# Performance work log

Measured on AMD Instinct MI355X. Metric: run time of the kernel, lower is better.

The kernel has to match this reference:

```python
import jax, jax.numpy as jnp
import numpy as np

B, N, F_IN, OUT_FEATS, NUM_CLS, NUM_INDS = 256, 200, 200, 256, 8, 512
PCT_EDGES = 20
K = int(PCT_EDGES / 100 * N * (N - 1) / 2)  # 3980 hard edges
TAU = 1.0


def setup_inputs() -> dict:
    key = jax.random.key(0)
    ks = jax.random.split(key, 6)
    x = jax.random.normal(ks[0], (B, N, F_IN), dtype=jnp.float32)
    gumbel_u = jax.random.uniform(ks[1], (B, N, N), dtype=jnp.float32)
    nets = jax.random.normal(ks[2], (NUM_INDS, N, N), dtype=jnp.float32)
    w_gnn = jax.random.normal(ks[3], (F_IN, OUT_FEATS), dtype=jnp.float32) / np.sqrt(F_IN).astype(np.float32)
    w_lin = jax.random.normal(ks[4], (OUT_FEATS, NUM_CLS), dtype=jnp.float32) / np.sqrt(OUT_FEATS).astype(np.float32)
    b_lin = jnp.zeros((NUM_CLS,), dtype=jnp.float32)
    net_index = jax.random.randint(ks[5], (B,), 0, NUM_INDS)
    return {"x": x, "gumbel_u": gumbel_u, "nets": nets, "w_gnn": w_gnn,
            "w_lin": w_lin, "b_lin": b_lin, "net_index": net_index}


def _gumbel_softkmax(logits, u, k, tau):
    # logits: [B, N, N]; u: uniform(0,1) noise -> Gumbel(0,1) via -log(-log(u))
    b, n, _ = logits.shape
    g = -jnp.log(-jnp.log(jnp.clip(u, 1e-10, 1.0 - 1e-10)))
    g = (logits + g) / tau
    sym = (g + jnp.swapaxes(g, 1, 2)) * 0.5                      # symmetrize
    y_soft = jax.nn.softmax(sym.reshape(b, -1), axis=-1).reshape(b, n, n)
    upper_flat = jnp.triu(y_soft).reshape(b, -1)                 # upper tri incl. diag
    _, idx = jax.lax.top_k(upper_flat, k)                        # [B, k]
    y_hard = jnp.zeros_like(upper_flat).at[jnp.arange(b)[:, None], idx].set(1.0)
    y_hard = y_hard.reshape(b, n, n)
    diag = jnp.diagonal(y_hard, axis1=-2, axis2=-1)              # [B, N]
    eye = jnp.eye(n, dtype=y_hard.dtype)
    y_hard = y_hard + jnp.swapaxes(y_hard, 1, 2) - diag[:, :, None] * eye
    # straight-through estimator
    return y_hard - jax.lax.stop_gradient(y_soft) + y_soft


def reference(x, gumbel_u, nets, w_gnn, w_lin, b_lin, net_index):
    selected = nets[net_index]                                   # [B, N, N]
    adj = _gumbel_softkmax(selected, gumbel_u, K, TAU)
    # gnn: relu(adj @ x @ W_gnn)  -> embeddings [B, N, OUT_FEATS]
    emb = jax.nn.relu(jnp.einsum('bij,bjf,fo->bio', adj, x, w_gnn))
    out = emb @ w_lin + b_lin                                    # [B, N, NUM_CLS]
    return out, emb, adj
```

## Files before the change

### kernel.cpp

```cpp
#include <hip/hip_runtime.h>
#include <math.h>

#define B_SZ 256
#define N_SZ 200
#define NN (N_SZ * N_SZ)
#define FIN 200
#define OUT_F 256
#define NCLS 8
#define KSEL 3980
#define NUPPER 20100
#define KSTRIDE 20128
#define NT 7
#define NTILES 28
#define CAND_CAP 2048

#define ADJ_STRIDE 224
#define KGRP_PB 25
#define XWM_PB (KGRP_PB * 2048)

#define EMB_OFF (B_SZ * N_SZ * NCLS)
#define ADJ_OFF (EMB_OFF + B_SZ * N_SZ * OUT_F)

#define KEYS_OFF_B   0
#define SEL_OFF_B    21659648
#define CCNT_OFF_B   21661696
#define CAND_OFF_B   21662720
#define WKG_OFF_B    26214400
#define ADJB16_OFF_B 26329088

typedef unsigned short ushort_t;
typedef float f32x4 __attribute__((ext_vector_type(4)));
typedef short bf16x8 __attribute__((ext_vector_type(8)));

__device__ __forceinline__ unsigned sortkey(float f) {
    unsigned u = __float_as_uint(f);
    return (u & 0x80000000u) ? ~u : (u | 0x80000000u);
}

__device__ __forceinline__ ushort_t f2b(float f) {
    unsigned u = __float_as_uint(f);
    return (ushort_t)((u + 0x7FFFu + ((u >> 16) & 1u)) >> 16);
}

__device__ __forceinline__ bf16x8 f2b8(float4 lo, float4 hi) {
    bf16x8 r;
    r[0] = (short)f2b(lo.x); r[1] = (short)f2b(lo.y);
    r[2] = (short)f2b(lo.z); r[3] = (short)f2b(lo.w);
    r[4] = (short)f2b(hi.x); r[5] = (short)f2b(hi.y);
    r[6] = (short)f2b(hi.z); r[7] = (short)f2b(hi.w);
    return r;
}

__device__ __forceinline__ void tile_decode(int t, int& ti, int& tj) {
    int a = 0, rem = t;
    while (rem >= NT - a) { rem -= NT - a; ++a; }
    ti = a; tj = a + rem;
}

__global__ __launch_bounds__(256) void kA(
    const float* __restrict__ gu, const float* __restrict__ nets,
    const int* __restrict__ net_index, unsigned* __restrict__ keys)
{
    const int blk = blockIdx.x;
    const int b = blk / NTILES;
    int ti, tj; tile_decode(blk % NTILES, ti, tj);
    const int i0 = ti * 32, j0 = tj * 32;
    const float* ub = gu + (size_t)b * NN;
    const float* lb = nets + (size_t)net_index[b] * NN;

    __shared__ float Hij[32][33];
    __shared__ float Hji[32][33];

    const int r = threadIdx.x >> 5;
    const int c = threadIdx.x & 31;

    #pragma unroll
    for (int s = 0; s < 4; ++s) {
        int rr = r + 8 * s;
        int i = i0 + rr, j = j0 + c;
        if (i < N_SZ && j < N_SZ) {
            float u = ub[i * N_SZ + j];
            u = fminf(fmaxf(u, 1e-10f), 1.0f - 1e-10f);
            Hij[rr][c] = lb[i * N_SZ + j] - logf(-logf(u));
        }
        if (ti != tj) {
            int i2 = j0 + rr, j2 = i0 + c;
            if (i2 < N_SZ && j2 < N_SZ) {
                float u = ub[i2 * N_SZ + j2];
                u = fminf(fmaxf(u, 1e-10f), 1.0f - 1e-10f);
                Hji[rr][c] = lb[i2 * N_SZ + j2] - logf(-logf(u));
            }
        }
    }
    __syncthreads();

    unsigned* kb = keys + (size_t)b * KSTRIDE;
    #pragma unroll
    for (int s = 0; s < 4; ++s) {
        int rr = r + 8 * s;
        int i = i0 + rr, j = j0 + c;
        if (i < N_SZ && j < N_SZ && i <= j) {
            float hji = (ti == tj) ? Hij[c][rr] : Hji[c][rr];
            float sv = 0.5f * (Hij[rr][c] + hji);
            int base = i * N_SZ - (i * (i - 1)) / 2;
            kb[base + (j - i)] = sortkey(sv);
        }
    }
}

__global__ __launch_bounds__(256) void kFinal(
    const unsigned* __restrict__ keys, unsigned* __restrict__ sel)
{
    const int b = blockIdx.x;
    const int tid = threadIdx.x;
    __shared__ unsigned kl[NUPPER];
    __shared__ unsigned hist[256];
    __shared__ unsigned sfx[256];
    __shared__ unsigned sPrefix;
    __shared__ int sKK;

    const unsigned* kb = keys + (size_t)b * KSTRIDE;
    for (int idx = tid; idx < NUPPER; idx += 256) kl[idx] = kb[idx];

    unsigned prefix = 0;
    int kk = KSEL;
    for (int round = 0; round < 4; ++round) {
        const int shift = 24 - 8 * round;
        hist[tid] = 0;
        __syncthreads();
        for (int idx = tid; idx < NUPPER; idx += 256) {
            unsigned key = kl[idx];
            bool in = (round == 0) || ((key >> (shift + 8)) == prefix);
            if (in) atomicAdd(&hist[(key >> shift) & 255u], 1u);
        }
        __syncthreads();
        sfx[tid] = hist[tid];
        __syncthreads();
        #pragma unroll
        for (int off = 1; off < 256; off <<= 1) {
            unsigned add = (tid + off < 256) ? sfx[tid + off] : 0u;
            __syncthreads();
            sfx[tid] += add;
            __syncthreads();
        }
        unsigned above = (tid < 255) ? sfx[tid + 1] : 0u;
        if (sfx[tid] >= (unsigned)kk && above < (unsigned)kk) {
            sPrefix = (prefix << 8) | (unsigned)tid;
            sKK = kk - (int)above;
        }
        __syncthreads();
        prefix = sPrefix;
        kk = sKK;
        __syncthreads();
    }
    if (tid == 0) {
        sel[b * 2] = prefix;
        sel[b * 2 + 1] = (unsigned)kk;
    }
}

__global__ __launch_bounds__(256) void kW(
    const unsigned* __restrict__ keys, const unsigned* __restrict__ sel,
    unsigned* __restrict__ candCnt, unsigned* __restrict__ cand,
    float* __restrict__ out_base, ushort_t* __restrict__ adjb16)
{
    const int blk = blockIdx.x;
    const int b = blk / NTILES;
    int ti, tj; tile_decode(blk % NTILES, ti, tj);
    const int i0 = ti * 32, j0 = tj * 32;
    const unsigned kth = sel[b * 2];
    const unsigned* kb = keys + (size_t)b * KSTRIDE;
    float* adj = out_base + ADJ_OFF + (size_t)b * NN;
    ushort_t* ab = adjb16 + (size_t)b * (N_SZ * ADJ_STRIDE);

    __shared__ float V[32][33];
    const int r = threadIdx.x >> 5;
    const int c = threadIdx.x & 31;

    #pragma unroll
    for (int s = 0; s < 4; ++s) {
        int rr = r + 8 * s;
        int i = i0 + rr, j = j0 + c;
        if (i < N_SZ && j < N_SZ && i <= j) {
            int base = i * N_SZ - (i * (i - 1)) / 2;
            unsigned key = kb[base + (j - i)];
            float v = (key > kth) ? 1.0f : 0.0f;
            if (key == kth) {
                unsigned p = atomicAdd(&candCnt[b], 1u);
                if (p < CAND_CAP) cand[(size_t)b * CAND_CAP + p] = (unsigned)(i * N_SZ + j);
            }
            V[rr][c] = v;
            if (ti == tj) V[c][rr] = v;
        }
    }
    __syncthreads();
    #pragma unroll
    for (int s = 0; s < 4; ++s) {
        int rr = r + 8 * s;
        int i = i0 + rr, j = j0 + c;
        if (i < N_SZ) {
            float v = (j < N_SZ) ? V[rr][c] : 0.0f;
            if (j < N_SZ) adj[i * N_SZ + j] = v;
            ab[i * ADJ_STRIDE + j] = (v != 0.0f) ? (ushort_t)0x3F80 : (ushort_t)0;
        }
    }
    if (ti != tj) {
        #pragma unroll
        for (int s = 0; s < 4; ++s) {
            int rr = r + 8 * s;
            int i2 = j0 + rr, j2 = i0 + c;
            if (i2 < N_SZ) {
                float v = V[c][rr];
                adj[i2 * N_SZ + j2] = v;
                ab[i2 * ADJ_STRIDE + j2] = (v != 0.0f) ? (ushort_t)0x3F80 : (ushort_t)0;
            }
        }
    }
}

__global__ void kT(const unsigned* __restrict__ sel,
                   const unsigned* __restrict__ candCnt,
                   const unsigned* __restrict__ cand,
                   float* __restrict__ out_base, ushort_t* __restrict__ adjb16)
{
    const int b = blockIdx.x;
    if (threadIdx.x != 0) return;
    int kk = (int)sel[b * 2 + 1];
    int cnt = (int)candCnt[b];
    if (cnt > CAND_CAP) cnt = CAND_CAP;
    float* adj = out_base + ADJ_OFF + (size_t)b * NN;
    ushort_t* ab = adjb16 + (size_t)b * (N_SZ * ADJ_STRIDE);
    int take = kk < cnt ? kk : cnt;
    unsigned used[64];
    int nu = 0;
    for (int t = 0; t < take; ++t) {
        unsigned best = 0xFFFFFFFFu;
        for (int q = 0; q < cnt; ++q) {
            unsigned v = cand[(size_t)b * CAND_CAP + q];
            bool skip = false;
            for (int u = 0; u < nu; ++u) if (used[u] == v) { skip = true; break; }
            if (!skip && v < best) best = v;
        }
        if (best == 0xFFFFFFFFu) break;
        if (nu < 64) used[nu++] = best;
        int i = (int)(best / N_SZ), j = (int)(best % N_SZ);
        adj[i * N_SZ + j] = 1.0f;
        adj[j * N_SZ + i] = 1.0f;
        ab[i * ADJ_STRIDE + j] = (ushort_t)0x3F80;
        ab[j * ADJ_STRIDE + i] = (ushort_t)0x3F80;
    }
}

__global__ __launch_bounds__(256) void kWprep(
    const float* __restrict__ wg, ushort_t* __restrict__ wkg,
    unsigned* __restrict__ candCnt)
{
    if (blockIdx.x == 0) candCnt[threadIdx.x] = 0;
    int e = blockIdx.x * 256 + threadIdx.x;
    int kg = e >> 11;
    int rem = e & 2047;
    int n = rem >> 3;
    int ki = rem & 7;
    int k = kg * 8 + ki;
    wkg[e] = (k < FIN) ? f2b(wg[k * OUT_F + n]) : (ushort_t)0;
}

__global__ __launch_bounds__(256) void k2_mfma(
    const float* __restrict__ x, const ushort_t* __restrict__ wkg,
    ushort_t* __restrict__ xwm)
{
    const int r0 = blockIdx.x * 64;
    const int tid = threadIdx.x;
    const int w = tid >> 6;
    const int l = tid & 63;
    const int g = l >> 4;
    const int r = l & 15;

    __shared__ __align__(16) ushort_t Cs[64 * 256];

    f32x4 acc[4][4];
    #pragma unroll
    for (int mf = 0; mf < 4; ++mf)
        #pragma unroll
        for (int nf = 0; nf < 4; ++nf)
            acc[mf][nf] = (f32x4){0.f, 0.f, 0.f, 0.f};

    for (int c = 0; c < 7; ++c) {
        const int koff = (c * 32 + g * 8 < FIN) ? (c * 32 + g * 8) : 0;
        bf16x8 af[4], bf[4];
        #pragma unroll
        for (int mf = 0; mf < 4; ++mf) {
            const float* ap = x + (size_t)(r0 + mf * 16 + r) * FIN + koff;
            float4 lo = *(const float4*)ap;
            float4 hi = *(const float4*)(ap + 4);
            af[mf] = f2b8(lo, hi);
        }
        #pragma unroll
        for (int nf = 0; nf < 4; ++nf)
            bf[nf] = *(const bf16x8*)(wkg + c * 8192 + g * 2048 + (w * 64 + nf * 16 + r) * 8);
        #pragma unroll
        for (int mf = 0; mf < 4; ++mf)
            #pragma unroll
            for (int nf = 0; nf < 4; ++nf)
                acc[mf][nf] = __builtin_amdgcn_mfma_f32_16x16x32_bf16(
                    af[mf], bf[nf], acc[mf][nf], 0, 0, 0);
    }

    #pragma unroll
    for (int mf = 0; mf < 4; ++mf) {
        #pragma unroll
        for (int jj = 0; jj < 4; ++jj) {
            int row = mf * 16 + g * 4 + jj;
            #pragma unroll
            for (int nf = 0; nf < 4; ++nf) {
                int col = w * 64 + nf * 16 + r;
                Cs[((row >> 3) << 11) + col * 8 + (row & 7)] = f2b(acc[mf][nf][jj]);
            }
        }
    }
    __syncthreads();
    #pragma unroll
    for (int kg = 0; kg < 8; ++kg) {
        int grow0 = r0 + kg * 8;
        int bb = grow0 / N_SZ;
        int jb = grow0 % N_SZ;
        ushort_t* dst = xwm + (size_t)bb * XWM_PB + ((jb >> 3) << 11);
        *(int4*)(dst + tid * 8) = *(const int4*)(Cs + (kg << 11) + tid * 8);
    }
}

__global__ __launch_bounds__(256) void k3_fused(
    const ushort_t* __restrict__ adjb16, const ushort_t* __restrict__ xwm,
    const float* __restrict__ wl, const float* __restrict__ bl,
    float* __restrict__ out_base)
{
    const int blk = blockIdx.x;
    const int xcd = blk & 7;
    const int idx = blk >> 3;
    const int b = xcd + 8 * (idx / 7);
    const int mt = idx % 7;
    const int tid = threadIdx.x;
    const int w = tid >> 6;
    const int l = tid & 63;
    const int g = l >> 4;
    const int r = l & 15;

    const ushort_t* adjb = adjb16 + (size_t)b * (N_SZ * ADJ_STRIDE);
    const ushort_t* xwb = xwm + (size_t)b * XWM_PB;

    __shared__ float red[4][4][8][8];

    int arow0 = mt * 32 + r;       if (arow0 > N_SZ - 1) arow0 = N_SZ - 1;
    int arow1 = mt * 32 + 16 + r;  if (arow1 > N_SZ - 1) arow1 = N_SZ - 1;
    bf16x8 aa[2][7];
    #pragma unroll
    for (int c = 0; c < 7; ++c) {
        aa[0][c] = *(const bf16x8*)(adjb + arow0 * ADJ_STRIDE + c * 32 + g * 8);
        aa[1][c] = *(const bf16x8*)(adjb + arow1 * ADJ_STRIDE + c * 32 + g * 8);
    }

    f32x4 acc[2][4];
    #pragma unroll
    for (int mf = 0; mf < 2; ++mf)
        #pragma unroll
        for (int nf = 0; nf < 4; ++nf)
            acc[mf][nf] = (f32x4){0.f, 0.f, 0.f, 0.f};

    #pragma unroll
    for (int c = 0; c < 7; ++c) {
        bf16x8 bf[4];
        #pragma unroll
        for (int nf = 0; nf < 4; ++nf)
            bf[nf] = *(const bf16x8*)(xwb + c * 8192 + g * 2048 + (w * 64 + nf * 16 + r) * 8);
        #pragma unroll
        for (int mf = 0; mf < 2; ++mf)
            #pragma unroll
            for (int nf = 0; nf < 4; ++nf)
                acc[mf][nf] = __builtin_amdgcn_mfma_f32_16x16x32_bf16(
                    aa[mf][c], bf[nf], acc[mf][nf], 0, 0, 0);
    }

    float wlv[4][NCLS];
    #pragma unroll
    for (int nf = 0; nf < 4; ++nf) {
        int col = w * 64 + nf * 16 + r;
        #pragma unroll
        for (int cls = 0; cls < NCLS; ++cls) wlv[nf][cls] = wl[col * NCLS + cls];
    }

    #pragma unroll
    for (int mf = 0; mf < 2; ++mf) {
        #pragma unroll
        for (int j = 0; j < 4; ++j) {
            int rowl = mf * 16 + g * 4 + j;
            int grow = mt * 32 + rowl;
            float e0 = fmaxf(acc[mf][0][j], 0.0f);
            float e1 = fmaxf(acc[mf][1][j], 0.0f);
            float e2 = fmaxf(acc[mf][2][j], 0.0f);
            float e3 = fmaxf(acc[mf][3][j], 0.0f);
            if (grow < N_SZ) {
                size_t rbase = EMB_OFF + ((size_t)b * N_SZ + grow) * OUT_F;
                out_base[rbase + w * 64 + r]      = e0;
                out_base[rbase + w * 64 + 16 + r] = e1;
                out_base[rbase + w * 64 + 32 + r] = e2;
                out_base[rbase + w * 64 + 48 + r] = e3;
            }
            float pr[NCLS];
            #pragma unroll
            for (int cls = 0; cls < NCLS; ++cls)
                pr[cls] = e0 * wlv[0][cls] + e1 * wlv[1][cls]
                        + e2 * wlv[2][cls] + e3 * wlv[3][cls];
            #pragma unroll
            for (int off = 1; off <= 8; off <<= 1) {
                #pragma unroll
                for (int cls = 0; cls < NCLS; ++cls)
                    pr[cls] += __shfl_xor(pr[cls], off, 64);
            }
            if (r < NCLS) red[w][g][mf * 4 + j][r] = pr[r];
        }
    }
    __syncthreads();

    {
        int rowl = tid >> 3, cls = tid & 7;
        int mf = rowl >> 4, rem = rowl & 15, gg = rem >> 2, jj = rem & 3;
        int slot = mf * 4 + jj;
        int grow = mt * 32 + rowl;
        if (grow < N_SZ) {
            float s = red[0][gg][slot][cls] + red[1][gg][slot][cls]
                    + red[2][gg][slot][cls] + red[3][gg][slot][cls] + bl[cls];
            out_base[((size_t)b * N_SZ + grow) * NCLS + cls] = s;
        }
    }
}

extern "C" void kernel_launch(void* const* d_in, const int* in_sizes, int n_in,
                              void* d_out, int out_size, void* d_ws, size_t ws_size,
                              hipStream_t stream) {
    const float* x    = (const float*)d_in[0];
    const float* gu   = (const float*)d_in[1];
    const float* nets = (const float*)d_in[2];
    const float* wg   = (const float*)d_in[3];
    const float* wl   = (const float*)d_in[4];
    const float* bl   = (const float*)d_in[5];
    const int*   nidx = (const int*)d_in[6];
    float* out = (float*)d_out;

    char* ws = (char*)d_ws;
    unsigned* keys    = (unsigned*)(ws + KEYS_OFF_B);
    unsigned* sel     = (unsigned*)(ws + SEL_OFF_B);
    unsigned* candCnt = (unsigned*)(ws + CCNT_OFF_B);
    unsigned* cand    = (unsigned*)(ws + CAND_OFF_B);
    ushort_t* xwm     = (ushort_t*)(ws + KEYS_OFF_B);
    ushort_t* wkg     = (ushort_t*)(ws + WKG_OFF_B);
    ushort_t* adjb16  = (ushort_t*)(ws + ADJB16_OFF_B);

    kWprep<<<224, 256, 0, stream>>>(wg, wkg, candCnt);
    kA<<<B_SZ * NTILES, 256, 0, stream>>>(gu, nets, nidx, keys);
    kFinal<<<B_SZ, 256, 0, stream>>>(keys, sel);
    kW<<<B_SZ * NTILES, 256, 0, stream>>>(keys, sel, candCnt, cand, out, adjb16);
    kT<<<B_SZ, 64, 0, stream>>>(sel, candCnt, cand, out, adjb16);

    k2_mfma<<<(B_SZ * N_SZ) / 64, 256, 0, stream>>>(x, wkg, xwm);
    k3_fused<<<B_SZ * 7, 256, 0, stream>>>(adjb16, xwm, wl, bl, out);
}
```

Before: 153.3 us.

## Fuse weight prep into kA, vectorize adjacency writes, stage embedding stores via LDS

```diff
diff --git a/kernel.cpp b/kernel.cpp
--- a/kernel.cpp
+++ b/kernel.cpp
@@ -31,6 +31,7 @@
 typedef unsigned short ushort_t;
 typedef float f32x4 __attribute__((ext_vector_type(4)));
 typedef short bf16x8 __attribute__((ext_vector_type(8)));
+typedef ushort_t u16x4 __attribute__((ext_vector_type(4)));
 
 __device__ __forceinline__ unsigned sortkey(float f) {
     unsigned u = __float_as_uint(f);
@@ -59,9 +60,23 @@
 
 __global__ __launch_bounds__(256) void kA(
     const float* __restrict__ gu, const float* __restrict__ nets,
-    const int* __restrict__ net_index, unsigned* __restrict__ keys)
+    const int* __restrict__ net_index, unsigned* __restrict__ keys,
+    const float* __restrict__ wg, ushort_t* __restrict__ wkg,
+    unsigned* __restrict__ candCnt)
 {
     const int blk = blockIdx.x;
+    if (blk >= B_SZ * NTILES) {
+        int pb = blk - B_SZ * NTILES;
+        if (pb == 0) candCnt[threadIdx.x] = 0;
+        int e = pb * 256 + threadIdx.x;
+        int kg = e >> 11;
+        int rem = e & 2047;
+        int n = rem >> 3;
+        int ki = rem & 7;
+        int k = kg * 8 + ki;
+        wkg[e] = (k < FIN) ? f2b(wg[k * OUT_F + n]) : (ushort_t)0;
+        return;
+    }
     const int b = blk / NTILES;
     int ti, tj; tile_decode(blk % NTILES, ti, tj);
     const int i0 = ti * 32, j0 = tj * 32;
@@ -194,26 +209,49 @@
         }
     }
     __syncthreads();
-    #pragma unroll
-    for (int s = 0; s < 4; ++s) {
-        int rr = r + 8 * s;
-        int i = i0 + rr, j = j0 + c;
+
+    const int tr = threadIdx.x >> 3;
+    const int tc = threadIdx.x & 7;
+    {
+        int i = i0 + tr;
         if (i < N_SZ) {
-            float v = (j < N_SZ) ? V[rr][c] : 0.0f;
-            if (j < N_SZ) adj[i * N_SZ + j] = v;
-            ab[i * ADJ_STRIDE + j] = (v != 0.0f) ? (ushort_t)0x3F80 : (ushort_t)0;
+            int jb = j0 + tc * 4;
+            float v0 = (jb + 0 < N_SZ) ? V[tr][tc * 4 + 0] : 0.0f;
+            float v1 = (jb + 1 < N_SZ) ? V[tr][tc * 4 + 1] : 0.0f;
+            float v2 = (jb + 2 < N_SZ) ? V[tr][tc * 4 + 2] : 0.0f;
+            float v3 = (jb + 3 < N_SZ) ? V[tr][tc * 4 + 3] : 0.0f;
+            if (jb + 3 < N_SZ) {
+                float4 v4 = {v0, v1, v2, v3};
+                *(float4*)(adj + (size_t)i * N_SZ + jb) = v4;
+            } else {
+                if (jb + 0 < N_SZ) adj[(size_t)i * N_SZ + jb + 0] = v0;
+                if (jb + 1 < N_SZ) adj[(size_t)i * N_SZ + jb + 1] = v1;
+                if (jb + 2 < N_SZ) adj[(size_t)i * N_SZ + jb + 2] = v2;
+            }
+            u16x4 a4;
+            a4[0] = (v0 != 0.0f) ? (ushort_t)0x3F80 : (ushort_t)0;
+            a4[1] = (v1 != 0.0f) ? (ushort_t)0x3F80 : (ushort_t)0;
+            a4[2] = (v2 != 0.0f) ? (ushort_t)0x3F80 : (ushort_t)0;
+            a4[3] = (v3 != 0.0f) ? (ushort_t)0x3F80 : (ushort_t)0;
+            *(u16x4*)(ab + (size_t)i * ADJ_STRIDE + jb) = a4;
         }
     }
     if (ti != tj) {
-        #pragma unroll
-        for (int s = 0; s < 4; ++s) {
-            int rr = r + 8 * s;
-            int i2 = j0 + rr, j2 = i0 + c;
-            if (i2 < N_SZ) {
-                float v = V[c][rr];
-                adj[i2 * N_SZ + j2] = v;
-                ab[i2 * ADJ_STRIDE + j2] = (v != 0.0f) ? (ushort_t)0x3F80 : (ushort_t)0;
-            }
+        int i2 = j0 + tr;
+        if (i2 < N_SZ) {
+            int jb = i0 + tc * 4;
+            float v0 = V[tc * 4 + 0][tr];
+            float v1 = V[tc * 4 + 1][tr];
+            float v2 = V[tc * 4 + 2][tr];
+            float v3 = V[tc * 4 + 3][tr];
+            float4 v4 = {v0, v1, v2, v3};
+            *(float4*)(adj + (size_t)i2 * N_SZ + jb) = v4;
+            u16x4 a4;
+            a4[0] = (v0 != 0.0f) ? (ushort_t)0x3F80 : (ushort_t)0;
+            a4[1] = (v1 != 0.0f) ? (ushort_t)0x3F80 : (ushort_t)0;
+            a4[2] = (v2 != 0.0f) ? (ushort_t)0x3F80 : (ushort_t)0;
+            a4[3] = (v3 != 0.0f) ? (ushort_t)0x3F80 : (ushort_t)0;
+            *(u16x4*)(ab + (size_t)i2 * ADJ_STRIDE + jb) = a4;
         }
     }
 }
@@ -251,20 +289,6 @@
     }
 }
 
-__global__ __launch_bounds__(256) void kWprep(
-    const float* __restrict__ wg, ushort_t* __restrict__ wkg,
-    unsigned* __restrict__ candCnt)
-{
-    if (blockIdx.x == 0) candCnt[threadIdx.x] = 0;
-    int e = blockIdx.x * 256 + threadIdx.x;
-    int kg = e >> 11;
-    int rem = e & 2047;
-    int n = rem >> 3;
-    int ki = rem & 7;
-    int k = kg * 8 + ki;
-    wkg[e] = (k < FIN) ? f2b(wg[k * OUT_F + n]) : (ushort_t)0;
-}
-
 __global__ __launch_bounds__(256) void k2_mfma(
     const float* __restrict__ x, const ushort_t* __restrict__ wkg,
     ushort_t* __restrict__ xwm)
@@ -348,7 +372,8 @@
     const ushort_t* adjb = adjb16 + (size_t)b * (N_SZ * ADJ_STRIDE);
     const ushort_t* xwb = xwm + (size_t)b * XWM_PB;
 
-    __shared__ float red[4][4][8][8];
+    __shared__ __align__(16) float Es[32 * 256];
+    float (*red)[4][8][8] = (float(*)[4][8][8])Es;
 
     int arow0 = mt * 32 + r;       if (arow0 > N_SZ - 1) arow0 = N_SZ - 1;
     int arow1 = mt * 32 + 16 + r;  if (arow1 > N_SZ - 1) arow1 = N_SZ - 1;
@@ -380,6 +405,30 @@
                     aa[mf][c], bf[nf], acc[mf][nf], 0, 0, 0);
     }
 
+    #pragma unroll
+    for (int mf = 0; mf < 2; ++mf) {
+        #pragma unroll
+        for (int j = 0; j < 4; ++j) {
+            int rowl = mf * 16 + g * 4 + j;
+            #pragma unroll
+            for (int nf = 0; nf < 4; ++nf)
+                Es[rowl * 256 + w * 64 + nf * 16 + r] = fmaxf(acc[mf][nf][j], 0.0f);
+        }
+    }
+    __syncthreads();
+    #pragma unroll
+    for (int q = 0; q < 8; ++q) {
+        int e = q * 256 + tid;
+        int rowl = e >> 6;
+        int c4 = e & 63;
+        int grow = mt * 32 + rowl;
+        if (grow < N_SZ) {
+            float4 v = *(const float4*)(Es + rowl * 256 + c4 * 4);
+            *(float4*)(out_base + EMB_OFF + ((size_t)b * N_SZ + grow) * OUT_F + c4 * 4) = v;
+        }
+    }
+    __syncthreads();
+
     float wlv[4][NCLS];
     #pragma unroll
     for (int nf = 0; nf < 4; ++nf) {
@@ -387,24 +436,14 @@
         #pragma unroll
         for (int cls = 0; cls < NCLS; ++cls) wlv[nf][cls] = wl[col * NCLS + cls];
     }
-
     #pragma unroll
     for (int mf = 0; mf < 2; ++mf) {
         #pragma unroll
         for (int j = 0; j < 4; ++j) {
-            int rowl = mf * 16 + g * 4 + j;
-            int grow = mt * 32 + rowl;
             float e0 = fmaxf(acc[mf][0][j], 0.0f);
             float e1 = fmaxf(acc[mf][1][j], 0.0f);
             float e2 = fmaxf(acc[mf][2][j], 0.0f);
             float e3 = fmaxf(acc[mf][3][j], 0.0f);
-            if (grow < N_SZ) {
-                size_t rbase = EMB_OFF + ((size_t)b * N_SZ + grow) * OUT_F;
-                out_base[rbase + w * 64 + r]      = e0;
-                out_base[rbase + w * 64 + 16 + r] = e1;
-                out_base[rbase + w * 64 + 32 + r] = e2;
-                out_base[rbase + w * 64 + 48 + r] = e3;
-            }
             float pr[NCLS];
             #pragma unroll
             for (int cls = 0; cls < NCLS; ++cls)
@@ -455,8 +494,7 @@
     ushort_t* wkg     = (ushort_t*)(ws + WKG_OFF_B);
     ushort_t* adjb16  = (ushort_t*)(ws + ADJB16_OFF_B);
 
-    kWprep<<<224, 256, 0, stream>>>(wg, wkg, candCnt);
-    kA<<<B_SZ * NTILES, 256, 0, stream>>>(gu, nets, nidx, keys);
+    kA<<<B_SZ * NTILES + 224, 256, 0, stream>>>(gu, nets, nidx, keys, wg, wkg, candCnt);
     kFinal<<<B_SZ, 256, 0, stream>>>(keys, sel);
     kW<<<B_SZ * NTILES, 256, 0, stream>>>(keys, sel, candCnt, cand, out, adjb16);
     kT<<<B_SZ, 64, 0, stream>>>(sel, candCnt, cand, out, adjb16);
```

Result: faster. 148.4 us (-3.2%).

## Fuse top-k selection with adjacency write and shrink GNN tiles

Applied to the files above, without the earlier changes.

```diff
diff --git a/kernel.cpp b/kernel.cpp
--- a/kernel.cpp
+++ b/kernel.cpp
@@ -12,7 +12,6 @@
 #define KSTRIDE 20128
 #define NT 7
 #define NTILES 28
-#define CAND_CAP 2048
 
 #define ADJ_STRIDE 224
 #define KGRP_PB 25
@@ -22,15 +21,14 @@
 #define ADJ_OFF (EMB_OFF + B_SZ * N_SZ * OUT_F)
 
 #define KEYS_OFF_B   0
-#define SEL_OFF_B    21659648
-#define CCNT_OFF_B   21661696
-#define CAND_OFF_B   21662720
 #define WKG_OFF_B    26214400
 #define ADJB16_OFF_B 26329088
 
 typedef unsigned short ushort_t;
 typedef float f32x4 __attribute__((ext_vector_type(4)));
 typedef short bf16x8 __attribute__((ext_vector_type(8)));
+typedef ushort_t u16x4 __attribute__((ext_vector_type(4)));
+typedef ushort_t u16x8 __attribute__((ext_vector_type(8)));
 
 __device__ __forceinline__ unsigned sortkey(float f) {
     unsigned u = __float_as_uint(f);
@@ -59,9 +57,21 @@
 
 __global__ __launch_bounds__(256) void kA(
     const float* __restrict__ gu, const float* __restrict__ nets,
-    const int* __restrict__ net_index, unsigned* __restrict__ keys)
+    const int* __restrict__ net_index, unsigned* __restrict__ keys,
+    const float* __restrict__ wg, ushort_t* __restrict__ wkg)
 {
     const int blk = blockIdx.x;
+    if (blk >= B_SZ * NTILES) {
+        int pb = blk - B_SZ * NTILES;
+        int e = pb * 256 + threadIdx.x;
+        int kg = e >> 11;
+        int rem = e & 2047;
+        int n = rem >> 3;
+        int ki = rem & 7;
+        int k = kg * 8 + ki;
+        wkg[e] = (k < FIN) ? f2b(wg[k * OUT_F + n]) : (ushort_t)0;
+        return;
+    }
     const int b = blk / NTILES;
     int ti, tj; tile_decode(blk % NTILES, ti, tj);
     const int i0 = ti * 32, j0 = tj * 32;
@@ -108,161 +118,121 @@
     }
 }
 
-__global__ __launch_bounds__(256) void kFinal(
-    const unsigned* __restrict__ keys, unsigned* __restrict__ sel)
+__global__ __launch_bounds__(512) void kSelW(
+    const unsigned* __restrict__ keys, float* __restrict__ out_base,
+    ushort_t* __restrict__ adjb16)
 {
     const int b = blockIdx.x;
     const int tid = threadIdx.x;
-    __shared__ unsigned kl[NUPPER];
+    __shared__ __align__(16) unsigned kl[NUPPER];
     __shared__ unsigned hist[256];
     __shared__ unsigned sfx[256];
+    __shared__ unsigned scanA[512];
     __shared__ unsigned sPrefix;
     __shared__ int sKK;
 
-    const unsigned* kb = keys + (size_t)b * KSTRIDE;
-    for (int idx = tid; idx < NUPPER; idx += 256) kl[idx] = kb[idx];
+    {
+        const int4* kb4 = (const int4*)(keys + (size_t)b * KSTRIDE);
+        int4* kl4 = (int4*)kl;
+        for (int q = tid; q < 5025; q += 512) kl4[q] = kb4[q];
+    }
 
     unsigned prefix = 0;
     int kk = KSEL;
     for (int round = 0; round < 4; ++round) {
         const int shift = 24 - 8 * round;
-        hist[tid] = 0;
-        __syncthreads();
-        for (int idx = tid; idx < NUPPER; idx += 256) {
+        if (tid < 256) hist[tid] = 0;
+        __syncthreads();
+        for (int idx = tid; idx < NUPPER; idx += 512) {
             unsigned key = kl[idx];
             bool in = (round == 0) || ((key >> (shift + 8)) == prefix);
             if (in) atomicAdd(&hist[(key >> shift) & 255u], 1u);
         }
         __syncthreads();
-        sfx[tid] = hist[tid];
+        if (tid < 256) sfx[tid] = hist[tid];
         __syncthreads();
         #pragma unroll
         for (int off = 1; off < 256; off <<= 1) {
-            unsigned add = (tid + off < 256) ? sfx[tid + off] : 0u;
+            unsigned add = 0;
+            if (tid < 256 && tid + off < 256) add = sfx[tid + off];
             __syncthreads();
-            sfx[tid] += add;
+            if (tid < 256) sfx[tid] += add;
             __syncthreads();
         }
-        unsigned above = (tid < 255) ? sfx[tid + 1] : 0u;
-        if (sfx[tid] >= (unsigned)kk && above < (unsigned)kk) {
-            sPrefix = (prefix << 8) | (unsigned)tid;
-            sKK = kk - (int)above;
+        if (tid < 256) {
+            unsigned above = (tid < 255) ? sfx[tid + 1] : 0u;
+            if (sfx[tid] >= (unsigned)kk && above < (unsigned)kk) {
+                sPrefix = (prefix << 8) | (unsigned)tid;
+                sKK = kk - (int)above;
+            }
         }
         __syncthreads();
         prefix = sPrefix;
         kk = sKK;
         __syncthreads();
     }
-    if (tid == 0) {
-        sel[b * 2] = prefix;
-        sel[b * 2 + 1] = (unsigned)kk;
-    }
-}
-
-__global__ __launch_bounds__(256) void kW(
-    const unsigned* __restrict__ keys, const unsigned* __restrict__ sel,
-    unsigned* __restrict__ candCnt, unsigned* __restrict__ cand,
-    float* __restrict__ out_base, ushort_t* __restrict__ adjb16)
-{
-    const int blk = blockIdx.x;
-    const int b = blk / NTILES;
-    int ti, tj; tile_decode(blk % NTILES, ti, tj);
-    const int i0 = ti * 32, j0 = tj * 32;
-    const unsigned kth = sel[b * 2];
-    const unsigned* kb = keys + (size_t)b * KSTRIDE;
+    const unsigned kth = prefix;
+
+    const int lo = tid * 40;
+    const int hi = (lo + 40 < NUPPER) ? lo + 40 : NUPPER;
+    unsigned mycnt = 0;
+    for (int idx = lo; idx < hi; ++idx)
+        if (kl[idx] == kth) ++mycnt;
+    scanA[tid] = mycnt;
+    __syncthreads();
+    #pragma unroll
+    for (int off = 1; off < 512; off <<= 1) {
+        unsigned add = (tid >= off) ? scanA[tid - off] : 0u;
+        __syncthreads();
+        scanA[tid] += add;
+        __syncthreads();
+    }
+    unsigned rank = scanA[tid] - mycnt;
+    for (int idx = lo; idx < hi; ++idx) {
+        unsigned key = kl[idx];
+        unsigned dec;
+        if (key > kth) dec = 1u;
+        else if (key == kth) { dec = (rank < (unsigned)kk) ? 1u : 0u; ++rank; }
+        else dec = 0u;
+        kl[idx] = dec;
+    }
+    __syncthreads();
+
     float* adj = out_base + ADJ_OFF + (size_t)b * NN;
+    for (int e = tid; e < 10000; e += 512) {
+        int i = e / 50;
+        int j0 = (e % 50) * 4;
+        int bi = i * N_SZ - (i * (i - 1)) / 2 - i;
+        float4 v;
+        float* vp = (float*)&v;
+        #pragma unroll
+        for (int q = 0; q < 4; ++q) {
+            int j = j0 + q;
+            int pk = (i <= j) ? (bi + j)
+                              : (j * N_SZ - (j * (j - 1)) / 2 + (i - j));
+            vp[q] = kl[pk] ? 1.0f : 0.0f;
+        }
+        *(float4*)(adj + (size_t)i * N_SZ + j0) = v;
+    }
     ushort_t* ab = adjb16 + (size_t)b * (N_SZ * ADJ_STRIDE);
-
-    __shared__ float V[32][33];
-    const int r = threadIdx.x >> 5;
-    const int c = threadIdx.x & 31;
-
-    #pragma unroll
-    for (int s = 0; s < 4; ++s) {
-        int rr = r + 8 * s;
-        int i = i0 + rr, j = j0 + c;
-        if (i < N_SZ && j < N_SZ && i <= j) {
-            int base = i * N_SZ - (i * (i - 1)) / 2;
-            unsigned key = kb[base + (j - i)];
-            float v = (key > kth) ? 1.0f : 0.0f;
-            if (key == kth) {
-                unsigned p = atomicAdd(&candCnt[b], 1u);
-                if (p < CAND_CAP) cand[(size_t)b * CAND_CAP + p] = (unsigned)(i * N_SZ + j);
+    for (int e = tid; e < 5600; e += 512) {
+        int i = e / 28;
+        int j0 = (e % 28) * 8;
+        int bi = i * N_SZ - (i * (i - 1)) / 2 - i;
+        u16x8 v;
+        #pragma unroll
+        for (int q = 0; q < 8; ++q) {
+            int j = j0 + q;
+            ushort_t o = 0;
+            if (j < N_SZ) {
+                int pk = (i <= j) ? (bi + j)
+                                  : (j * N_SZ - (j * (j - 1)) / 2 + (i - j));
+                o = kl[pk] ? (ushort_t)0x3F80 : (ushort_t)0;
             }
-            V[rr][c] = v;
-            if (ti == tj) V[c][rr] = v;
-        }
-    }
-    __syncthreads();
-    #pragma unroll
-    for (int s = 0; s < 4; ++s) {
-        int rr = r + 8 * s;
-        int i = i0 + rr, j = j0 + c;
-        if (i < N_SZ) {
-            float v = (j < N_SZ) ? V[rr][c] : 0.0f;
-            if (j < N_SZ) adj[i * N_SZ + j] = v;
-            ab[i * ADJ_STRIDE + j] = (v != 0.0f) ? (ushort_t)0x3F80 : (ushort_t)0;
-        }
-    }
-    if (ti != tj) {
-        #pragma unroll
-        for (int s = 0; s < 4; ++s) {
-            int rr = r + 8 * s;
-            int i2 = j0 + rr, j2 = i0 + c;
-            if (i2 < N_SZ) {
-                float v = V[c][rr];
-                adj[i2 * N_SZ + j2] = v;
-                ab[i2 * ADJ_STRIDE + j2] = (v != 0.0f) ? (ushort_t)0x3F80 : (ushort_t)0;
-            }
-        }
-    }
-}
-
-__global__ void kT(const unsigned* __restrict__ sel,
-                   const unsigned* __restrict__ candCnt,
-                   const unsigned* __restrict__ cand,
-                   float* __restrict__ out_base, ushort_t* __restrict__ adjb16)
-{
-    const int b = blockIdx.x;
-    if (threadIdx.x != 0) return;
-    int kk = (int)sel[b * 2 + 1];
-    int cnt = (int)candCnt[b];
-    if (cnt > CAND_CAP) cnt = CAND_CAP;
-    float* adj = out_base + ADJ_OFF + (size_t)b * NN;
-    ushort_t* ab = adjb16 + (size_t)b * (N_SZ * ADJ_STRIDE);
-    int take = kk < cnt ? kk : cnt;
-    unsigned used[64];
-    int nu = 0;
-    for (int t = 0; t < take; ++t) {
-        unsigned best = 0xFFFFFFFFu;
-        for (int q = 0; q < cnt; ++q) {
-            unsigned v = cand[(size_t)b * CAND_CAP + q];
-            bool skip = false;
-            for (int u = 0; u < nu; ++u) if (used[u] == v) { skip = true; break; }
-            if (!skip && v < best) best = v;
-        }
-        if (best == 0xFFFFFFFFu) break;
-        if (nu < 64) used[nu++] = best;
-        int i = (int)(best / N_SZ), j = (int)(best % N_SZ);
-        adj[i * N_SZ + j] = 1.0f;
-        adj[j * N_SZ + i] = 1.0f;
-        ab[i * ADJ_STRIDE + j] = (ushort_t)0x3F80;
-        ab[j * ADJ_STRIDE + i] = (ushort_t)0x3F80;
-    }
-}
-
-__global__ __launch_bounds__(256) void kWprep(
-    const float* __restrict__ wg, ushort_t* __restrict__ wkg,
-    unsigned* __restrict__ candCnt)
-{
-    if (blockIdx.x == 0) candCnt[threadIdx.x] = 0;
-    int e = blockIdx.x * 256 + threadIdx.x;
-    int kg = e >> 11;
-    int rem = e & 2047;
-    int n = rem >> 3;
-    int ki = rem & 7;
-    int k = kg * 8 + ki;
-    wkg[e] = (k < FIN) ? f2b(wg[k * OUT_F + n]) : (ushort_t)0;
+            v[q] = o;
+        }
+        *(u16x8*)(ab + (size_t)i * ADJ_STRIDE + j0) = v;
+    }
 }
 
 __global__ __launch_bounds__(256) void k2_mfma(
@@ -337,8 +307,8 @@
     const int blk = blockIdx.x;
     const int xcd = blk & 7;
     const int idx = blk >> 3;
-    const int b = xcd + 8 * (idx / 7);
-    const int mt = idx % 7;
+    const int b = xcd + 8 * (idx / 13);
+    const int mt = idx % 13;
     const int tid = threadIdx.x;
     const int w = tid >> 6;
     const int l = tid & 63;
@@ -348,23 +318,18 @@
     const ushort_t* adjb = adjb16 + (size_t)b * (N_SZ * ADJ_STRIDE);
     const ushort_t* xwb = xwm + (size_t)b * XWM_PB;
 
-    __shared__ float red[4][4][8][8];
-
-    int arow0 = mt * 32 + r;       if (arow0 > N_SZ - 1) arow0 = N_SZ - 1;
-    int arow1 = mt * 32 + 16 + r;  if (arow1 > N_SZ - 1) arow1 = N_SZ - 1;
-    bf16x8 aa[2][7];
-    #pragma unroll
-    for (int c = 0; c < 7; ++c) {
-        aa[0][c] = *(const bf16x8*)(adjb + arow0 * ADJ_STRIDE + c * 32 + g * 8);
-        aa[1][c] = *(const bf16x8*)(adjb + arow1 * ADJ_STRIDE + c * 32 + g * 8);
-    }
-
-    f32x4 acc[2][4];
-    #pragma unroll
-    for (int mf = 0; mf < 2; ++mf)
-        #pragma unroll
-        for (int nf = 0; nf < 4; ++nf)
-            acc[mf][nf] = (f32x4){0.f, 0.f, 0.f, 0.f};
+    __shared__ __align__(16) float Es[16 * 256];
+    float (*red)[4][4][8] = (float(*)[4][4][8])Es;
+
+    int arow = mt * 16 + r; if (arow > N_SZ - 1) arow = N_SZ - 1;
+    bf16x8 aa[7];
+    #pragma unroll
+    for (int c = 0; c < 7; ++c)
+        aa[c] = *(const bf16x8*)(adjb + arow * ADJ_STRIDE + c * 32 + g * 8);
+
+    f32x4 acc[4];
+    #pragma unroll
+    for (int nf = 0; nf < 4; ++nf) acc[nf] = (f32x4){0.f, 0.f, 0.f, 0.f};
 
     #pragma unroll
     for (int c = 0; c < 7; ++c) {
@@ -373,12 +338,31 @@
         for (int nf = 0; nf < 4; ++nf)
             bf[nf] = *(const bf16x8*)(xwb + c * 8192 + g * 2048 + (w * 64 + nf * 16 + r) * 8);
         #pragma unroll
-        for (int mf = 0; mf < 2; ++mf)
-            #pragma unroll
-            for (int nf = 0; nf < 4; ++nf)
-                acc[mf][nf] = __builtin_amdgcn_mfma_f32_16x16x32_bf16(
-                    aa[mf][c], bf[nf], acc[mf][nf], 0, 0, 0);
-    }
+        for (int nf = 0; nf < 4; ++nf)
+            acc[nf] = __builtin_amdgcn_mfma_f32_16x16x32_bf16(
+                aa[c], bf[nf], acc[nf], 0, 0, 0);
+    }
+
+    #pragma unroll
+    for (int j = 0; j < 4; ++j) {
+        int rowl = g * 4 + j;
+        #pragma unroll
+        for (int nf = 0; nf < 4; ++nf)
+            Es[rowl * 256 + w * 64 + nf * 16 + r] = fmaxf(acc[nf][j], 0.0f);
+    }
+    __syncthreads();
+    #pragma unroll
+    for (int q = 0; q < 4; ++q) {
+        int e = q * 256 + tid;
+        int rowl = e >> 6;
+        int c4 = e & 63;
+        int grow = mt * 16 + rowl;
+        if (grow < N_SZ) {
+            float4 v = *(const float4*)(Es + rowl * 256 + c4 * 4);
+            *(float4*)(out_base + EMB_OFF + ((size_t)b * N_SZ + grow) * OUT_F + c4 * 4) = v;
+        }
+    }
+    __syncthreads();
 
     float wlv[4][NCLS];
     #pragma unroll
@@ -387,48 +371,34 @@
         #pragma unroll
         for (int cls = 0; cls < NCLS; ++cls) wlv[nf][cls] = wl[col * NCLS + cls];
     }
-
-    #pragma unroll
-    for (int mf = 0; mf < 2; ++mf) {
-        #pragma unroll
-        for (int j = 0; j < 4; ++j) {
-            int rowl = mf * 16 + g * 4 + j;
-            int grow = mt * 32 + rowl;
-            float e0 = fmaxf(acc[mf][0][j], 0.0f);
-            float e1 = fmaxf(acc[mf][1][j], 0.0f);
-            float e2 = fmaxf(acc[mf][2][j], 0.0f);
-            float e3 = fmaxf(acc[mf][3][j], 0.0f);
-            if (grow < N_SZ) {
-                size_t rbase = EMB_OFF + ((size_t)b * N_SZ + grow) * OUT_F;
-                out_base[rbase + w * 64 + r]      = e0;
-                out_base[rbase + w * 64 + 16 + r] = e1;
-                out_base[rbase + w * 64 + 32 + r] = e2;
-                out_base[rbase + w * 64 + 48 + r] = e3;
-            }
-            float pr[NCLS];
+    #pragma unroll
+    for (int j = 0; j < 4; ++j) {
+        float e0 = fmaxf(acc[0][j], 0.0f);
+        float e1 = fmaxf(acc[1][j], 0.0f);
+        float e2 = fmaxf(acc[2][j], 0.0f);
+        float e3 = fmaxf(acc[3][j], 0.0f);
+        float pr[NCLS];
+        #pragma unroll
+        for (int cls = 0; cls < NCLS; ++cls)
+            pr[cls] = e0 * wlv[0][cls] + e1 * wlv[1][cls]
+                    + e2 * wlv[2][cls] + e3 * wlv[3][cls];
+        #pragma unroll
+        for (int off = 1; off <= 8; off <<= 1) {
             #pragma unroll
             for (int cls = 0; cls < NCLS; ++cls)
-                pr[cls] = e0 * wlv[0][cls] + e1 * wlv[1][cls]
-                        + e2 * wlv[2][cls] + e3 * wlv[3][cls];
-            #pragma unroll
-            for (int off = 1; off <= 8; off <<= 1) {
-                #pragma unroll
-                for (int cls = 0; cls < NCLS; ++cls)
-                    pr[cls] += __shfl_xor(pr[cls], off, 64);
-            }
-            if (r < NCLS) red[w][g][mf * 4 + j][r] = pr[r];
-        }
-    }
-    __syncthreads();
-
-    {
+                pr[cls] += __shfl_xor(pr[cls], off, 64);
+        }
+        if (r < NCLS) red[w][g][j][r] = pr[r];
+    }
+    __syncthreads();
+
+    if (tid < 16 * NCLS) {
         int rowl = tid >> 3, cls = tid & 7;
-        int mf = rowl >> 4, rem = rowl & 15, gg = rem >> 2, jj = rem & 3;
-        int slot = mf * 4 + jj;
-        int grow = mt * 32 + rowl;
+        int gg = rowl >> 2, jj = rowl & 3;
+        int grow = mt * 16 + rowl;
         if (grow < N_SZ) {
-            float s = red[0][gg][slot][cls] + red[1][gg][slot][cls]
-                    + red[2][gg][slot][cls] + red[3][gg][slot][cls] + bl[cls];
+            float s = red[0][gg][jj][cls] + red[1][gg][jj][cls]
+                    + red[2][gg][jj][cls] + red[3][gg][jj][cls] + bl[cls];
             out_base[((size_t)b * N_SZ + grow) * NCLS + cls] = s;
         }
     }
@@ -448,19 +418,12 @@
 
     char* ws = (char*)d_ws;
     unsigned* keys    = (unsigned*)(ws + KEYS_OFF_B);
-    unsigned* sel     = (unsigned*)(ws + SEL_OFF_B);
-    unsigned* candCnt = (unsigned*)(ws + CCNT_OFF_B);
-    unsigned* cand    = (unsigned*)(ws + CAND_OFF_B);
     ushort_t* xwm     = (ushort_t*)(ws + KEYS_OFF_B);
     ushort_t* wkg     = (ushort_t*)(ws + WKG_OFF_B);
     ushort_t* adjb16  = (ushort_t*)(ws + ADJB16_OFF_B);
 
-    kWprep<<<224, 256, 0, stream>>>(wg, wkg, candCnt);
-    kA<<<B_SZ * NTILES, 256, 0, stream>>>(gu, nets, nidx, keys);
-    kFinal<<<B_SZ, 256, 0, stream>>>(keys, sel);
-    kW<<<B_SZ * NTILES, 256, 0, stream>>>(keys, sel, candCnt, cand, out, adjb16);
-    kT<<<B_SZ, 64, 0, stream>>>(sel, candCnt, cand, out, adjb16);
-
+    kA<<<B_SZ * NTILES + 224, 256, 0, stream>>>(gu, nets, nidx, keys, wg, wkg);
+    kSelW<<<B_SZ, 512, 0, stream>>>(keys, out, adjb16);
     k2_mfma<<<(B_SZ * N_SZ) / 64, 256, 0, stream>>>(x, wkg, xwm);
-    k3_fused<<<B_SZ * 7, 256, 0, stream>>>(adjb16, xwm, wl, bl, out);
-}
+    k3_fused<<<B_SZ * 13, 256, 0, stream>>>(adjb16, xwm, wl, bl, out);
+}
```

New measurement: 149.5 us. 1.03x faster.
